# Performance work log

Hardware: AMD Instinct MI355X
Metric: run time of the kernel (lower is better)

Reference implementation:

```python
import jax, jax.numpy as jnp
import numpy as np

N = 50000
E = 400000
IN_DIM = 128
HID = 128
OUT = 128
HEADS = 4
NEG_SLOPE = 0.2
EPS = 1e-16


def setup_inputs() -> dict:
    key = jax.random.key(0)
    ks = jax.random.split(key, 12)
    s = 0.05
    return {
        "x": jax.random.normal(ks[0], (N, IN_DIM), dtype=jnp.float32),
        "edge_index": jax.random.randint(ks[1], (2, E), 0, N, dtype=jnp.int64),
        # layer 1: in_dim -> hid, heads=4, concat
        "W1": jax.random.normal(ks[2], (IN_DIM, HEADS * HID), dtype=jnp.float32) * s,
        "att_src1": jax.random.normal(ks[3], (HEADS, HID), dtype=jnp.float32) * s,
        "att_dst1": jax.random.normal(ks[4], (HEADS, HID), dtype=jnp.float32) * s,
        "bias1": jnp.zeros((HEADS * HID,), dtype=jnp.float32),
        # layer 2: hid*heads -> out, heads=1, no concat
        "W2": jax.random.normal(ks[5], (HEADS * HID, OUT), dtype=jnp.float32) * s,
        "att_src2": jax.random.normal(ks[6], (1, OUT), dtype=jnp.float32) * s,
        "att_dst2": jax.random.normal(ks[7], (1, OUT), dtype=jnp.float32) * s,
        "bias2": jnp.zeros((OUT,), dtype=jnp.float32),
    }


def gat_conv(x, src, dst, W, att_src, att_dst, bias, heads, out_dim, concat):
    n = x.shape[0]
    h = (x @ W).reshape(n, heads, out_dim)                       # [N,H,D]
    a_src = jnp.sum(h * att_src[None], axis=-1)                  # [N,H]
    a_dst = jnp.sum(h * att_dst[None], axis=-1)                  # [N,H]
    e = jax.nn.leaky_relu(a_src[src] + a_dst[dst], NEG_SLOPE)    # [E,H]
    # segment softmax over incoming edges of each dst node
    e_max = jax.ops.segment_max(e, dst, num_segments=n)          # [N,H]
    ex = jnp.exp(e - e_max[dst])
    denom = jax.ops.segment_sum(ex, dst, num_segments=n)         # [N,H]
    alpha = ex / (denom[dst] + EPS)                              # [E,H]
    msg = h[src] * alpha[..., None]                              # [E,H,D]
    out = jax.ops.segment_sum(msg, dst, num_segments=n)          # [N,H,D]
    out = out.reshape(n, heads * out_dim) if concat else out.mean(axis=1)
    return out + bias


def reference(x, edge_index, W1, att_src1, att_dst1, bias1, W2, att_src2, att_dst2, bias2):
    n = x.shape[0]
    loop = jnp.arange(n, dtype=edge_index.dtype)
    src = jnp.concatenate([edge_index[0], loop])  # PyG add_self_loops=True
    dst = jnp.concatenate([edge_index[1], loop])
    h = jax.nn.elu(gat_conv(x, src, dst, W1, att_src1, att_dst1, bias1, HEADS, HID, True))
    z = jax.nn.elu(gat_conv(h, src, dst, W2, att_src2, att_dst2, bias2, 1, OUT, False))
    # F.normalize(z, dim=-1): L2 with eps=1e-12 clamp on the norm
    norm = jnp.maximum(jnp.linalg.norm(z, axis=-1, keepdims=True), 1e-12)
    return z / norm
```

## Files before the change

kernel.cpp:

```cpp
#include <hip/hip_runtime.h>
#include <cstddef>

#define N_NODES 50000
#define N_EDGES 400000
#define TOT_EDGES (N_EDGES + N_NODES)
#define M_PAD 50048
#define SCAN_PAD 50176
#define NBLK 49
#define CNT_BLKS 1758

typedef _Float16 f16;
typedef __attribute__((ext_vector_type(8))) _Float16 f16x8;
typedef __attribute__((ext_vector_type(4))) _Float16 f16x4;
typedef __attribute__((ext_vector_type(2))) _Float16 f16x2;
typedef __attribute__((ext_vector_type(4))) float f32x4;

__device__ __forceinline__ float lrelu(float e) { return e > 0.f ? e : 0.2f * e; }

__global__ void zero_int(int* __restrict__ p, int n) {
  int i = blockIdx.x * blockDim.x + threadIdx.x;
  if (i < n) p[i] = 0;
}

__global__ __launch_bounds__(256) void count_weights(
    const int* __restrict__ ei, int* __restrict__ deg,
    const float* __restrict__ W1, const float* __restrict__ W2,
    const float* __restrict__ att_s1, const float* __restrict__ att_d1,
    const float* __restrict__ att_s2, const float* __restrict__ att_d2,
    f16* __restrict__ w1t, f16* __restrict__ w2t,
    float* __restrict__ V1s, float* __restrict__ V1d,
    float* __restrict__ V2s, float* __restrict__ V2d) {
  const int b = blockIdx.x;
  if (b < CNT_BLKS) {
    const int e = b * 256 + threadIdx.x;
    if (e >= TOT_EDGES) return;
    const int dst = (e < N_EDGES) ? ei[N_EDGES + e] : (e - N_EDGES);
    atomicAdd(&deg[dst], 1);
    return;
  }
  const int bb = b - CNT_BLKS;
  if (bb < 256) {
    const int idx = bb * 256 + threadIdx.x;
    const int cc = idx >> 7, rr = idx & 127;
    w1t[idx] = (f16)W1[(size_t)rr * 512 + cc];
  } else if (bb < 512) {
    const int idx = (bb - 256) * 256 + threadIdx.x;
    const int cc = idx >> 9, rr = idx & 511;
    w2t[idx] = (f16)W2[(size_t)rr * 128 + cc];
  } else if (bb < 640) {
    const int wid = (bb - 512) * 4 + (threadIdx.x >> 6);
    const int lane = threadIdx.x & 63;
    const int k = wid >> 2, h = wid & 3;
    const float* wrow = W1 + (size_t)k * 512 + h * 128;
    float2 wv = *(const float2*)&wrow[lane * 2];
    float2 sv = *(const float2*)&att_s1[h * 128 + lane * 2];
    float2 dv = *(const float2*)&att_d1[h * 128 + lane * 2];
    float ps = wv.x * sv.x + wv.y * sv.y;
    float pd = wv.x * dv.x + wv.y * dv.y;
#pragma unroll
    for (int off = 32; off; off >>= 1) {
      ps += __shfl_xor(ps, off);
      pd += __shfl_xor(pd, off);
    }
    if (lane == 0) { V1s[k * 4 + h] = ps; V1d[k * 4 + h] = pd; }
  } else {
    const int wid = (bb - 640) * 4 + (threadIdx.x >> 6);
    const int lane = threadIdx.x & 63;
    const float* wrow = W2 + (size_t)wid * 128;
    float2 wv = *(const float2*)&wrow[lane * 2];
    float2 sv = *(const float2*)&att_s2[lane * 2];
    float2 dv = *(const float2*)&att_d2[lane * 2];
    float ps = wv.x * sv.x + wv.y * sv.y;
    float pd = wv.x * dv.x + wv.y * dv.y;
#pragma unroll
    for (int off = 32; off; off >>= 1) {
      ps += __shfl_xor(ps, off);
      pd += __shfl_xor(pd, off);
    }
    if (lane == 0) { V2s[wid] = ps; V2d[wid] = pd; }
  }
}

__global__ __launch_bounds__(256) void histscan_prepx(
    const int* __restrict__ deg, int* __restrict__ pre, int* __restrict__ bsum,
    int* __restrict__ blkcnt,
    const float* __restrict__ x, f16* __restrict__ xb,
    const float* __restrict__ V1s, const float* __restrict__ V1d,
    float* __restrict__ as1, float* __restrict__ ad1, f16* __restrict__ aggb) {
  __shared__ int wsum[4];
  __shared__ int lh[128];
  const int b = blockIdx.x;
  if (b < NBLK) {
    const int t = threadIdx.x, lane = t & 63, w = t >> 6;
    if (t < 128) lh[t] = 0;
    __syncthreads();
    const int base = b * 1024 + t * 4;
    int4 v = *(const int4*)&deg[base];
    if (base + 0 < N_NODES) atomicAdd(&lh[min(v.x, 127)], 1);
    if (base + 1 < N_NODES) atomicAdd(&lh[min(v.y, 127)], 1);
    if (base + 2 < N_NODES) atomicAdd(&lh[min(v.z, 127)], 1);
    if (base + 3 < N_NODES) atomicAdd(&lh[min(v.w, 127)], 1);
    const int s = v.x + v.y + v.z + v.w;
    int xx = s;
#pragma unroll
    for (int off = 1; off < 64; off <<= 1) {
      int y = __shfl_up(xx, off);
      if (lane >= off) xx += y;
    }
    if (lane == 63) wsum[w] = xx;
    __syncthreads();
    int woff = 0;
    for (int j = 0; j < w; ++j) woff += wsum[j];
    const int ex = xx - s + woff;
    pre[base + 0] = ex;
    pre[base + 1] = ex + v.x;
    pre[base + 2] = ex + v.x + v.y;
    pre[base + 3] = ex + v.x + v.y + v.z;
    if (t == 255) bsum[b] = ex + s;
    if (t < 128) blkcnt[t * NBLK + b] = lh[t];
    return;
  }
  const int wid = (b - NBLK) * 4 + (threadIdx.x >> 6);
  const int lane = threadIdx.x & 63;
  const int k = lane * 2;
  if (wid >= N_NODES) {
    f16x2 z; z[0] = (f16)0.f; z[1] = (f16)0.f;
    *(f16x2*)&xb[(size_t)wid * 128 + k] = z;
    f16x8 z8;
#pragma unroll
    for (int j = 0; j < 8; ++j) z8[j] = (f16)0.f;
    *(f16x8*)&aggb[(size_t)wid * 512 + lane * 8] = z8;
    return;
  }
  float2 xv = *(const float2*)&x[(size_t)wid * 128 + k];
  f16x2 o; o[0] = (f16)xv.x; o[1] = (f16)xv.y;
  *(f16x2*)&xb[(size_t)wid * 128 + k] = o;
  float4 vs0 = *(const float4*)&V1s[k * 4];
  float4 vs1 = *(const float4*)&V1s[(k + 1) * 4];
  float4 vd0 = *(const float4*)&V1d[k * 4];
  float4 vd1 = *(const float4*)&V1d[(k + 1) * 4];
  float s[4], d[4];
  s[0] = xv.x * vs0.x + xv.y * vs1.x;
  s[1] = xv.x * vs0.y + xv.y * vs1.y;
  s[2] = xv.x * vs0.z + xv.y * vs1.z;
  s[3] = xv.x * vs0.w + xv.y * vs1.w;
  d[0] = xv.x * vd0.x + xv.y * vd1.x;
  d[1] = xv.x * vd0.y + xv.y * vd1.y;
  d[2] = xv.x * vd0.z + xv.y * vd1.z;
  d[3] = xv.x * vd0.w + xv.y * vd1.w;
#pragma unroll
  for (int h = 0; h < 4; ++h) {
#pragma unroll
    for (int off = 32; off; off >>= 1) {
      s[h] += __shfl_xor(s[h], off);
      d[h] += __shfl_xor(d[h], off);
    }
  }
  if (lane == 0) {
    *(float4*)&as1[(size_t)wid * 4] = make_float4(s[0], s[1], s[2], s[3]);
    *(float4*)&ad1[(size_t)wid * 4] = make_float4(d[0], d[1], d[2], d[3]);
  }
}

__global__ __launch_bounds__(128) void scan2(int* __restrict__ bsum,
                                             const int* __restrict__ blkcnt,
                                             int* __restrict__ boff) {
  __shared__ int tot[128];
  const int t = threadIdx.x;
  int s = 0;
  for (int k = 0; k < NBLK; ++k) s += blkcnt[t * NBLK + k];
  tot[t] = s;
  __syncthreads();
  if (t == 0) {
    int acc = 0;
    for (int b = 0; b < 128; ++b) { const int v = tot[b]; tot[b] = acc; acc += v; }
  }
  __syncthreads();
  int acc = tot[t];
  for (int k = 0; k < NBLK; ++k) {
    boff[t * NBLK + k] = acc;
    acc += blkcnt[t * NBLK + k];
  }
  if (t < 64) {
    int v = (t < NBLK) ? bsum[t] : 0;
    int xx = v;
#pragma unroll
    for (int off = 1; off < 64; off <<= 1) {
      int y = __shfl_up(xx, off);
      if (t >= off) xx += y;
    }
    if (t < NBLK) bsum[t] = xx - v;
  }
}

__global__ __launch_bounds__(256) void scatter_addoff(
    int* __restrict__ pre, const int* __restrict__ bsumoff,
    int* __restrict__ cursor, const int* __restrict__ deg,
    const int* __restrict__ boff, int* __restrict__ order) {
  __shared__ int lcur[128];
  const int t = threadIdx.x;
  const int b = blockIdx.x;
  if (t < 128) lcur[t] = boff[t * NBLK + b];
  __syncthreads();
  const int base4 = b * 1024 + t * 4;
  const int off = bsumoff[b];
  int4 v = *(const int4*)&pre[base4];
  v.x += off; v.y += off; v.z += off; v.w += off;
  *(int4*)&pre[base4] = v;
  *(int4*)&cursor[base4] = v;
#pragma unroll
  for (int j = 0; j < 4; ++j) {
    const int i = b * 1024 + j * 256 + t;
    if (i < N_NODES) {
      const int bk = min(deg[i], 127);
      const int pos = atomicAdd(&lcur[bk], 1);
      order[pos] = i;
    }
  }
}

__global__ void fill_w1(const int* __restrict__ ei, int* __restrict__ cursor,
                        const float* __restrict__ as1, const float* __restrict__ ad1,
                        int* __restrict__ csr, float* __restrict__ wexp1) {
  const int e = blockIdx.x * blockDim.x + threadIdx.x;
  if (e >= TOT_EDGES) return;
  int s, d;
  if (e < N_EDGES) { s = ei[e]; d = ei[N_EDGES + e]; }
  else             { s = d = e - N_EDGES; }
  const int pos = atomicAdd(&cursor[d], 1);
  csr[pos] = s;
  float4 a = *(const float4*)&as1[(size_t)s * 4];
  float4 bz = *(const float4*)&ad1[(size_t)d * 4];
  float4 w;
  w.x = __expf(lrelu(a.x + bz.x));
  w.y = __expf(lrelu(a.y + bz.y));
  w.z = __expf(lrelu(a.z + bz.z));
  w.w = __expf(lrelu(a.w + bz.w));
  *(float4*)&wexp1[(size_t)pos * 4] = w;
}

template <int K, bool PER_HEAD, bool FUSE_A2>
__global__ __launch_bounds__(256) void gemm_bt(const f16* __restrict__ A, int lda,
                                               const f16* __restrict__ Bt, int ldb,
                                               f16* __restrict__ C, int ldc,
                                               const float* __restrict__ bias,
                                               const float* __restrict__ V2s,
                                               const float* __restrict__ V2d,
                                               float* __restrict__ as2,
                                               float* __restrict__ ad2) {
  if constexpr (PER_HEAD) {
    const int hh = blockIdx.y;
    A += (size_t)hh * 128;
    Bt += (size_t)hh * 128 * 128;
    C += (size_t)hh * 128;
    bias += hh * 128;
  }
  constexpr int LDT = 72;
  __shared__ __align__(16) f16 As[128 * LDT];
  __shared__ __align__(16) f16 Bs[128 * LDT];
  const int tid = threadIdx.x;
  const int lane = tid & 63;
  const int g = lane >> 4, r16 = lane & 15;
  const int w = tid >> 6, wr = w >> 1, wc = w & 1;
  const long bm = (long)blockIdx.x * 128;

  const int row0 = tid >> 2, h0 = tid & 3;
  const int p1 = (h0 & 1) * 16 + (h0 >> 1) * 4;
  const size_t ga0 = (size_t)(bm + row0) * lda + h0 * 8;
  const size_t ga1 = (size_t)(bm + row0 + 64) * lda + h0 * 8;
  const size_t gb0 = (size_t)row0 * ldb + h0 * 8;
  const size_t gb1 = (size_t)(row0 + 64) * ldb + h0 * 8;
  const int la0 = row0 * LDT + p1, la1 = (row0 + 64) * LDT + p1;

  f32x4 acc[4][4] = {};
  float s2a = 0.f, d2a = 0.f, s2b = 0.f, d2b = 0.f;

  for (int k0 = 0; k0 < K; k0 += 64) {
    __syncthreads();
    f16x8 a0k0 = *(const f16x8*)&A[ga0 + k0];
    f16x8 a0k1 = *(const f16x8*)&A[ga0 + k0 + 32];
    f16x8 a1k0 = *(const f16x8*)&A[ga1 + k0];
    f16x8 a1k1 = *(const f16x8*)&A[ga1 + k0 + 32];
    f16x8 b0k0 = *(const f16x8*)&Bt[gb0 + k0];
    f16x8 b0k1 = *(const f16x8*)&Bt[gb0 + k0 + 32];
    f16x8 b1k0 = *(const f16x8*)&Bt[gb1 + k0];
    f16x8 b1k1 = *(const f16x8*)&Bt[gb1 + k0 + 32];
    if constexpr (FUSE_A2) {
#pragma unroll
      for (int c = 0; c < 2; ++c) {
        const int kc = k0 + c * 32 + h0 * 8;
        const f16x8 va = c ? a0k1 : a0k0;
        const f16x8 vb = c ? a1k1 : a1k0;
        float4 vsa = *(const float4*)&V2s[kc];
        float4 vsb = *(const float4*)&V2s[kc + 4];
        float4 vda = *(const float4*)&V2d[kc];
        float4 vdb = *(const float4*)&V2d[kc + 4];
        const float vs[8] = {vsa.x, vsa.y, vsa.z, vsa.w, vsb.x, vsb.y, vsb.z, vsb.w};
        const float vd[8] = {vda.x, vda.y, vda.z, vda.w, vdb.x, vdb.y, vdb.z, vdb.w};
#pragma unroll
        for (int j = 0; j < 8; ++j) {
          s2a += (float)va[j] * vs[j];
          d2a += (float)va[j] * vd[j];
          s2b += (float)vb[j] * vs[j];
          d2b += (float)vb[j] * vd[j];
        }
      }
    }
    *(f16x4*)&As[la0]      = __builtin_shufflevector(a0k0, a0k0, 0, 1, 2, 3);
    *(f16x4*)&As[la0 + 8]  = __builtin_shufflevector(a0k0, a0k0, 4, 5, 6, 7);
    *(f16x4*)&As[la0 + 32] = __builtin_shufflevector(a0k1, a0k1, 0, 1, 2, 3);
    *(f16x4*)&As[la0 + 40] = __builtin_shufflevector(a0k1, a0k1, 4, 5, 6, 7);
    *(f16x4*)&As[la1]      = __builtin_shufflevector(a1k0, a1k0, 0, 1, 2, 3);
    *(f16x4*)&As[la1 + 8]  = __builtin_shufflevector(a1k0, a1k0, 4, 5, 6, 7);
    *(f16x4*)&As[la1 + 32] = __builtin_shufflevector(a1k1, a1k1, 0, 1, 2, 3);
    *(f16x4*)&As[la1 + 40] = __builtin_shufflevector(a1k1, a1k1, 4, 5, 6, 7);
    *(f16x4*)&Bs[la0]      = __builtin_shufflevector(b0k0, b0k0, 0, 1, 2, 3);
    *(f16x4*)&Bs[la0 + 8]  = __builtin_shufflevector(b0k0, b0k0, 4, 5, 6, 7);
    *(f16x4*)&Bs[la0 + 32] = __builtin_shufflevector(b0k1, b0k1, 0, 1, 2, 3);
    *(f16x4*)&Bs[la0 + 40] = __builtin_shufflevector(b0k1, b0k1, 4, 5, 6, 7);
    *(f16x4*)&Bs[la1]      = __builtin_shufflevector(b1k0, b1k0, 0, 1, 2, 3);
    *(f16x4*)&Bs[la1 + 8]  = __builtin_shufflevector(b1k0, b1k0, 4, 5, 6, 7);
    *(f16x4*)&Bs[la1 + 32] = __builtin_shufflevector(b1k1, b1k1, 0, 1, 2, 3);
    *(f16x4*)&Bs[la1 + 40] = __builtin_shufflevector(b1k1, b1k1, 4, 5, 6, 7);
    __syncthreads();
#pragma unroll
    for (int ks = 0; ks < 2; ++ks) {
      f16x8 af[4], bfv[4];
#pragma unroll
      for (int m = 0; m < 4; ++m)
        af[m] = *(const f16x8*)&As[(wr * 64 + m * 16 + r16) * LDT + ks * 32 + g * 8];
#pragma unroll
      for (int n = 0; n < 4; ++n)
        bfv[n] = *(const f16x8*)&Bs[(wc * 64 + n * 16 + r16) * LDT + ks * 32 + g * 8];
#pragma unroll
      for (int m = 0; m < 4; ++m)
#pragma unroll
        for (int n = 0; n < 4; ++n)
          acc[m][n] = __builtin_amdgcn_mfma_f32_16x16x32_f16(af[m], bfv[n], acc[m][n], 0, 0, 0);
    }
  }

  if constexpr (FUSE_A2) {
    s2a += __shfl_xor(s2a, 1); s2a += __shfl_xor(s2a, 2);
    d2a += __shfl_xor(d2a, 1); d2a += __shfl_xor(d2a, 2);
    s2b += __shfl_xor(s2b, 1); s2b += __shfl_xor(s2b, 2);
    d2b += __shfl_xor(d2b, 1); d2b += __shfl_xor(d2b, 2);
    if ((tid & 3) == 0) {
      const long r0 = bm + row0;
      as2[r0] = s2a; ad2[r0] = d2a;
      as2[r0 + 64] = s2b; ad2[r0 + 64] = d2b;
    }
  }

#pragma unroll
  for (int m = 0; m < 4; ++m) {
#pragma unroll
    for (int n = 0; n < 4; ++n) {
      const long row = bm + wr * 64 + m * 16 + g * 4;
      const int col = wc * 64 + n * 16 + r16;
      float bv = 0.f;
      if constexpr (PER_HEAD) bv = bias[col];
#pragma unroll
      for (int r = 0; r < 4; ++r) {
        float v = acc[m][n][r];
        if constexpr (PER_HEAD) {
          v += bv;
          v = v > 0.f ? v : (__expf(v) - 1.f);
        }
        C[(size_t)(row + r) * ldc + col] = (f16)v;
      }
    }
  }
}

__global__ __launch_bounds__(256) void aggregate1x(
    const f16* __restrict__ xsrc, const float* __restrict__ wexp,
    const int* __restrict__ rowstart, const int* __restrict__ csr,
    const int* __restrict__ order, f16* __restrict__ aggb) {
  const int wave = (blockIdx.x * blockDim.x + threadIdx.x) >> 6;
  const int lane = threadIdx.x & 63;
  const int g16 = lane >> 4, l16 = lane & 15;
  const int node = order[N_NODES - 1 - (wave * 4 + g16)];
  const int col0 = l16 * 8;
  const int rs = rowstart[node];
  const int re = rowstart[node + 1];
  const int deg = re - rs;

  int maxdeg = deg, mindeg = deg;
  maxdeg = max(maxdeg, __shfl_xor(maxdeg, 16));
  maxdeg = max(maxdeg, __shfl_xor(maxdeg, 32));
  mindeg = min(mindeg, __shfl_xor(mindeg, 16));
  mindeg = min(mindeg, __shfl_xor(mindeg, 32));

  constexpr int D = 4;
  int sreg[D];
  float4 wreg[D];
  f16x8 hreg[D];
#pragma unroll
  for (int p = 0; p < D; ++p) {
    const int k = rs + p;
    const int kc = (k < re) ? k : (re - 1);
    wreg[p] = *(const float4*)&wexp[(size_t)kc * 4];
    const int s = csr[kc];
    hreg[p] = *(const f16x8*)&xsrc[(size_t)s * 128 + col0];
    const int k2 = rs + D + p;
    sreg[p] = csr[(k2 < re) ? k2 : (re - 1)];
  }

  float acc0[8] = {}, acc1[8] = {}, acc2[8] = {}, acc3[8] = {};
  float Z0 = 0.f, Z1 = 0.f, Z2 = 0.f, Z3 = 0.f;

  int base = 0;
  for (; base + D <= mindeg; base += D) {
#pragma unroll
    for (int p = 0; p < D; ++p) {
      const int i = base + p;
      const float4 wv = wreg[p];
      const f16x8 h = hreg[p];
      const int nk = rs + i + D;
      if (nk < re) {
        wreg[p] = *(const float4*)&wexp[(size_t)nk * 4];
        const int s = sreg[p];
        hreg[p] = *(const f16x8*)&xsrc[(size_t)s * 128 + col0];
      }
      const int nk2 = rs + i + 2 * D;
      if (nk2 < re) sreg[p] = csr[nk2];
      Z0 += wv.x; Z1 += wv.y; Z2 += wv.z; Z3 += wv.w;
#pragma unroll
      for (int j = 0; j < 8; ++j) {
        const float hv = (float)h[j];
        acc0[j] += wv.x * hv;
        acc1[j] += wv.y * hv;
        acc2[j] += wv.z * hv;
        acc3[j] += wv.w * hv;
      }
    }
  }
  for (; base < maxdeg; base += D) {
#pragma unroll
    for (int p = 0; p < D; ++p) {
      const int i = base + p;
      const bool act = i < deg;
      const float4 wv = wreg[p];
      const float w0 = act ? wv.x : 0.f;
      const float w1 = act ? wv.y : 0.f;
      const float w2 = act ? wv.z : 0.f;
      const float w3 = act ? wv.w : 0.f;
      const f16x8 h = hreg[p];
      const int nk = rs + i + D;
      if (nk < re) {
        wreg[p] = *(const float4*)&wexp[(size_t)nk * 4];
        const int s = sreg[p];
        hreg[p] = *(const f16x8*)&xsrc[(size_t)s * 128 + col0];
      }
      const int nk2 = rs + i + 2 * D;
      if (nk2 < re) sreg[p] = csr[nk2];
      Z0 += w0; Z1 += w1; Z2 += w2; Z3 += w3;
#pragma unroll
      for (int j = 0; j < 8; ++j) {
        const float hv = (float)h[j];
        acc0[j] += w0 * hv;
        acc1[j] += w1 * hv;
        acc2[j] += w2 * hv;
        acc3[j] += w3 * hv;
      }
    }
  }

  const float i0 = 1.f / (Z0 + 1e-16f);
  const float i1 = 1.f / (Z1 + 1e-16f);
  const float i2 = 1.f / (Z2 + 1e-16f);
  const float i3 = 1.f / (Z3 + 1e-16f);
  f16* orow = aggb + (size_t)node * 512 + col0;
  f16x8 o0, o1, o2, o3;
#pragma unroll
  for (int j = 0; j < 8; ++j) {
    o0[j] = (f16)(acc0[j] * i0);
    o1[j] = (f16)(acc1[j] * i1);
    o2[j] = (f16)(acc2[j] * i2);
    o3[j] = (f16)(acc3[j] * i3);
  }
  *(f16x8*)&orow[0]   = o0;
  *(f16x8*)&orow[128] = o1;
  *(f16x8*)&orow[256] = o2;
  *(f16x8*)&orow[384] = o3;
}

__global__ __launch_bounds__(256) void aggregate2(
    const f16* __restrict__ hsrc, const float* __restrict__ as2,
    const float* __restrict__ ad2, const int* __restrict__ rowstart,
    const int* __restrict__ csr, const int* __restrict__ order,
    const float* __restrict__ bias, float* __restrict__ out) {
  const int wave = (blockIdx.x * blockDim.x + threadIdx.x) >> 6;
  const int lane = threadIdx.x & 63;
  const int g16 = lane >> 4, l16 = lane & 15;
  const int node = order[N_NODES - 1 - (wave * 4 + g16)];
  const int col0 = l16 * 8;
  const int rs = rowstart[node];
  const int re = rowstart[node + 1];
  const int deg = re - rs;
  const float ad = ad2[node];

  int maxdeg = deg, mindeg = deg;
  maxdeg = max(maxdeg, __shfl_xor(maxdeg, 16));
  maxdeg = max(maxdeg, __shfl_xor(maxdeg, 32));
  mindeg = min(mindeg, __shfl_xor(mindeg, 16));
  mindeg = min(mindeg, __shfl_xor(mindeg, 32));

  constexpr int D = 6;
  int sreg[D];
  float areg[D];
  f16x8 hreg[D];
#pragma unroll
  for (int p = 0; p < D; ++p) {
    const int k = rs + p;
    const int kc = (k < re) ? k : (re - 1);
    const int s = csr[kc];
    areg[p] = as2[s];
    hreg[p] = *(const f16x8*)&hsrc[(size_t)s * 128 + col0];
    const int k2 = rs + D + p;
    sreg[p] = csr[(k2 < re) ? k2 : (re - 1)];
  }

  float acc[8] = {};
  float Z = 0.f;
  int base = 0;
  for (; base + D <= mindeg; base += D) {
#pragma unroll
    for (int p = 0; p < D; ++p) {
      const int i = base + p;
      const float w = __expf(lrelu(areg[p] + ad));
      const f16x8 h = hreg[p];
      const int nk = rs + i + D;
      if (nk < re) {
        const int s = sreg[p];
        areg[p] = as2[s];
        hreg[p] = *(const f16x8*)&hsrc[(size_t)s * 128 + col0];
      }
      const int nk2 = rs + i + 2 * D;
      if (nk2 < re) sreg[p] = csr[nk2];
      Z += w;
#pragma unroll
      for (int j = 0; j < 8; ++j) acc[j] += w * (float)h[j];
    }
  }
  for (; base < maxdeg; base += D) {
#pragma unroll
    for (int p = 0; p < D; ++p) {
      const int i = base + p;
      const bool act = i < deg;
      const float w = act ? __expf(lrelu(areg[p] + ad)) : 0.f;
      const f16x8 h = hreg[p];
      const int nk = rs + i + D;
      if (nk < re) {
        const int s = sreg[p];
        areg[p] = as2[s];
        hreg[p] = *(const f16x8*)&hsrc[(size_t)s * 128 + col0];
      }
      const int nk2 = rs + i + 2 * D;
      if (nk2 < re) sreg[p] = csr[nk2];
      Z += w;
#pragma unroll
      for (int j = 0; j < 8; ++j) acc[j] += w * (float)h[j];
    }
  }
  const float inv = 1.f / (Z + 1e-16f);

  float4 ba = *(const float4*)&bias[col0];
  float4 bb = *(const float4*)&bias[col0 + 4];
  const float bv[8] = {ba.x, ba.y, ba.z, ba.w, bb.x, bb.y, bb.z, bb.w};
  float v[8];
  float ss = 0.f;
#pragma unroll
  for (int j = 0; j < 8; ++j) {
    float t = acc[j] * inv + bv[j];
    t = t > 0.f ? t : (__expf(t) - 1.f);
    v[j] = t;
    ss += t * t;
  }
  ss += __shfl_xor(ss, 1);
  ss += __shfl_xor(ss, 2);
  ss += __shfl_xor(ss, 4);
  ss += __shfl_xor(ss, 8);
  const float invn = 1.f / fmaxf(sqrtf(ss), 1e-12f);
  float* orow = out + (size_t)node * 128 + col0;
  float4 oa = make_float4(v[0] * invn, v[1] * invn, v[2] * invn, v[3] * invn);
  float4 ob = make_float4(v[4] * invn, v[5] * invn, v[6] * invn, v[7] * invn);
  *(float4*)&orow[0] = oa;
  *(float4*)&orow[4] = ob;
}

extern "C" void kernel_launch(void* const* d_in, const int* in_sizes, int n_in,
                              void* d_out, int out_size, void* d_ws, size_t ws_size,
                              hipStream_t stream) {
  const float* x        = (const float*)d_in[0];
  const int*   ei       = (const int*)d_in[1];
  const float* W1       = (const float*)d_in[2];
  const float* att_src1 = (const float*)d_in[3];
  const float* att_dst1 = (const float*)d_in[4];
  const float* bias1    = (const float*)d_in[5];
  const float* W2       = (const float*)d_in[6];
  const float* att_src2 = (const float*)d_in[7];
  const float* att_dst2 = (const float*)d_in[8];
  const float* bias2    = (const float*)d_in[9];
  float* out = (float*)d_out;

  char* ws = (char*)d_ws;
  size_t off = 0;
  auto alloc = [&](size_t bytes) {
    char* p = ws + off;
    off = (off + bytes + 255) & ~(size_t)255;
    return p;
  };
  f16* xb    = (f16*)alloc(sizeof(f16) * (size_t)M_PAD * 128);
  f16* w1t   = (f16*)alloc(sizeof(f16) * 512 * 128);
  f16* w2t   = (f16*)alloc(sizeof(f16) * 128 * 512);
  f16* aggb  = (f16*)alloc(sizeof(f16) * (size_t)M_PAD * 512);
  f16* out1b = (f16*)alloc(sizeof(f16) * (size_t)M_PAD * 512);
  float* V1s = (float*)alloc(sizeof(float) * 512);
  float* V1d = (float*)alloc(sizeof(float) * 512);
  float* V2s = (float*)alloc(sizeof(float) * 512);
  float* V2d = (float*)alloc(sizeof(float) * 512);
  float* as1 = (float*)alloc(sizeof(float) * N_NODES * 4);
  float* ad1 = (float*)alloc(sizeof(float) * N_NODES * 4);
  float* as2 = (float*)alloc(sizeof(float) * M_PAD);
  float* ad2 = (float*)alloc(sizeof(float) * M_PAD);
  float* wexp1 = (float*)alloc(sizeof(float) * (size_t)TOT_EDGES * 4);
  int* rowstart = (int*)alloc(sizeof(int) * (SCAN_PAD + 4));
  int* deg      = (int*)alloc(sizeof(int) * SCAN_PAD);
  int* cursor   = (int*)alloc(sizeof(int) * SCAN_PAD);
  int* bsum     = (int*)alloc(sizeof(int) * 64);
  int* blkcnt   = (int*)alloc(sizeof(int) * 128 * NBLK);
  int* boff     = (int*)alloc(sizeof(int) * 128 * NBLK);
  int* order    = (int*)alloc(sizeof(int) * N_NODES);
  int* csr      = (int*)alloc(sizeof(int) * TOT_EDGES);
  f16* h2b = aggb;

  const int agrid = (N_NODES / 4) * 64 / 256;

  zero_int<<<(SCAN_PAD + 255) / 256, 256, 0, stream>>>(deg, SCAN_PAD);
  count_weights<<<CNT_BLKS + 768, 256, 0, stream>>>(
      ei, deg, W1, W2, att_src1, att_dst1, att_src2, att_dst2,
      w1t, w2t, V1s, V1d, V2s, V2d);
  histscan_prepx<<<NBLK + M_PAD / 4, 256, 0, stream>>>(
      deg, rowstart, bsum, blkcnt, x, xb, V1s, V1d, as1, ad1, aggb);
  scan2<<<1, 128, 0, stream>>>(bsum, blkcnt, boff);
  scatter_addoff<<<NBLK, 256, 0, stream>>>(rowstart, bsum, cursor, deg, boff, order);
  fill_w1<<<CNT_BLKS, 256, 0, stream>>>(ei, cursor, as1, ad1, csr, wexp1);
  aggregate1x<<<agrid, 256, 0, stream>>>(xb, wexp1, rowstart, csr, order, aggb);
  gemm_bt<128, true, false><<<dim3(M_PAD / 128, 4), 256, 0, stream>>>(
      aggb, 512, w1t, 128, out1b, 512, bias1, nullptr, nullptr, nullptr, nullptr);
  gemm_bt<512, false, true><<<dim3(M_PAD / 128, 1), 256, 0, stream>>>(
      out1b, 512, w2t, 512, h2b, 128, nullptr, V2s, V2d, as2, ad2);
  aggregate2<<<agrid, 256, 0, stream>>>(h2b, as2, ad2, rowstart, csr, order, bias2, out);
}
```

Baseline: 192.1 us.

## Fuse the two GEMMs into one kernel and merge scan into scatter

```diff
diff --git a/kernel.cpp b/kernel.cpp
--- a/kernel.cpp
+++ b/kernel.cpp
@@ -11,7 +11,6 @@
 
 typedef _Float16 f16;
 typedef __attribute__((ext_vector_type(8))) _Float16 f16x8;
-typedef __attribute__((ext_vector_type(4))) _Float16 f16x4;
 typedef __attribute__((ext_vector_type(2))) _Float16 f16x2;
 typedef __attribute__((ext_vector_type(4))) float f32x4;
 
@@ -162,48 +161,40 @@
   }
 }
 
-__global__ __launch_bounds__(128) void scan2(int* __restrict__ bsum,
-                                             const int* __restrict__ blkcnt,
-                                             int* __restrict__ boff) {
-  __shared__ int tot[128];
-  const int t = threadIdx.x;
-  int s = 0;
-  for (int k = 0; k < NBLK; ++k) s += blkcnt[t * NBLK + k];
-  tot[t] = s;
-  __syncthreads();
-  if (t == 0) {
-    int acc = 0;
-    for (int b = 0; b < 128; ++b) { const int v = tot[b]; tot[b] = acc; acc += v; }
-  }
-  __syncthreads();
-  int acc = tot[t];
-  for (int k = 0; k < NBLK; ++k) {
-    boff[t * NBLK + k] = acc;
-    acc += blkcnt[t * NBLK + k];
-  }
-  if (t < 64) {
-    int v = (t < NBLK) ? bsum[t] : 0;
-    int xx = v;
-#pragma unroll
-    for (int off = 1; off < 64; off <<= 1) {
-      int y = __shfl_up(xx, off);
-      if (t >= off) xx += y;
-    }
-    if (t < NBLK) bsum[t] = xx - v;
-  }
-}
-
-__global__ __launch_bounds__(256) void scatter_addoff(
-    int* __restrict__ pre, const int* __restrict__ bsumoff,
+__global__ __launch_bounds__(256) void scatter_addoff2(
+    int* __restrict__ pre, const int* __restrict__ bsum,
     int* __restrict__ cursor, const int* __restrict__ deg,
-    const int* __restrict__ boff, int* __restrict__ order) {
+    const int* __restrict__ blkcnt, int* __restrict__ order) {
   __shared__ int lcur[128];
+  __shared__ int carry_s;
+  __shared__ int boff_s;
   const int t = threadIdx.x;
   const int b = blockIdx.x;
-  if (t < 128) lcur[t] = boff[t * NBLK + b];
+  int x = 0, tot = 0, pre_b = 0;
+  if (t < 128) {
+    for (int k = 0; k < NBLK; ++k) {
+      const int v = blkcnt[t * NBLK + k];
+      tot += v;
+      if (k < b) pre_b += v;
+    }
+    x = tot;
+#pragma unroll
+    for (int off = 1; off < 64; off <<= 1) {
+      int y = __shfl_up(x, off);
+      if ((t & 63) >= off) x += y;
+    }
+  }
+  if (t == 63) carry_s = x;
+  if (t == 255) {
+    int s = 0;
+    for (int k = 0; k < b; ++k) s += bsum[k];
+    boff_s = s;
+  }
+  __syncthreads();
+  if (t < 128) lcur[t] = (x - tot) + (t >= 64 ? carry_s : 0) + pre_b;
   __syncthreads();
   const int base4 = b * 1024 + t * 4;
-  const int off = bsumoff[b];
+  const int off = boff_s;
   int4 v = *(const int4*)&pre[base4];
   v.x += off; v.y += off; v.z += off; v.w += off;
   *(int4*)&pre[base4] = v;
@@ -239,138 +230,140 @@
   *(float4*)&wexp1[(size_t)pos * 4] = w;
 }
 
-template <int K, bool PER_HEAD, bool FUSE_A2>
-__global__ __launch_bounds__(256) void gemm_bt(const f16* __restrict__ A, int lda,
-                                               const f16* __restrict__ Bt, int ldb,
-                                               f16* __restrict__ C, int ldc,
-                                               const float* __restrict__ bias,
-                                               const float* __restrict__ V2s,
-                                               const float* __restrict__ V2d,
-                                               float* __restrict__ as2,
-                                               float* __restrict__ ad2) {
-  if constexpr (PER_HEAD) {
-    const int hh = blockIdx.y;
-    A += (size_t)hh * 128;
-    Bt += (size_t)hh * 128 * 128;
-    C += (size_t)hh * 128;
-    bias += hh * 128;
-  }
-  constexpr int LDT = 72;
-  __shared__ __align__(16) f16 As[128 * LDT];
-  __shared__ __align__(16) f16 Bs[128 * LDT];
+#define GLDT 72
+#define C1LD 136
+
+__global__ __launch_bounds__(256) void fused_mlp(
+    const f16* __restrict__ aggb, const f16* __restrict__ w1t,
+    const f16* __restrict__ w2t, const float* __restrict__ bias1,
+    const float* __restrict__ V2s, const float* __restrict__ V2d,
+    f16* __restrict__ h2b, float* __restrict__ as2, float* __restrict__ ad2) {
+  __shared__ __align__(16) f16 As[128 * GLDT];
+  __shared__ __align__(16) f16 Bs[128 * GLDT];
+  __shared__ __align__(16) f16 C1s[128 * C1LD];
+  __shared__ float a2sl[128], a2dl[128];
   const int tid = threadIdx.x;
   const int lane = tid & 63;
   const int g = lane >> 4, r16 = lane & 15;
   const int w = tid >> 6, wr = w >> 1, wc = w & 1;
-  const long bm = (long)blockIdx.x * 128;
-
+  const size_t bm = (size_t)blockIdx.x * 128;
   const int row0 = tid >> 2, h0 = tid & 3;
-  const int p1 = (h0 & 1) * 16 + (h0 >> 1) * 4;
-  const size_t ga0 = (size_t)(bm + row0) * lda + h0 * 8;
-  const size_t ga1 = (size_t)(bm + row0 + 64) * lda + h0 * 8;
-  const size_t gb0 = (size_t)row0 * ldb + h0 * 8;
-  const size_t gb1 = (size_t)(row0 + 64) * ldb + h0 * 8;
-  const int la0 = row0 * LDT + p1, la1 = (row0 + 64) * LDT + p1;
-
-  f32x4 acc[4][4] = {};
-  float s2a = 0.f, d2a = 0.f, s2b = 0.f, d2b = 0.f;
-
-  for (int k0 = 0; k0 < K; k0 += 64) {
-    __syncthreads();
-    f16x8 a0k0 = *(const f16x8*)&A[ga0 + k0];
-    f16x8 a0k1 = *(const f16x8*)&A[ga0 + k0 + 32];
-    f16x8 a1k0 = *(const f16x8*)&A[ga1 + k0];
-    f16x8 a1k1 = *(const f16x8*)&A[ga1 + k0 + 32];
-    f16x8 b0k0 = *(const f16x8*)&Bt[gb0 + k0];
-    f16x8 b0k1 = *(const f16x8*)&Bt[gb0 + k0 + 32];
-    f16x8 b1k0 = *(const f16x8*)&Bt[gb1 + k0];
-    f16x8 b1k1 = *(const f16x8*)&Bt[gb1 + k0 + 32];
-    if constexpr (FUSE_A2) {
-#pragma unroll
-      for (int c = 0; c < 2; ++c) {
-        const int kc = k0 + c * 32 + h0 * 8;
-        const f16x8 va = c ? a0k1 : a0k0;
-        const f16x8 vb = c ? a1k1 : a1k0;
-        float4 vsa = *(const float4*)&V2s[kc];
-        float4 vsb = *(const float4*)&V2s[kc + 4];
-        float4 vda = *(const float4*)&V2d[kc];
-        float4 vdb = *(const float4*)&V2d[kc + 4];
-        const float vs[8] = {vsa.x, vsa.y, vsa.z, vsa.w, vsb.x, vsb.y, vsb.z, vsb.w};
-        const float vd[8] = {vda.x, vda.y, vda.z, vda.w, vdb.x, vdb.y, vdb.z, vdb.w};
-#pragma unroll
-        for (int j = 0; j < 8; ++j) {
-          s2a += (float)va[j] * vs[j];
-          d2a += (float)va[j] * vd[j];
-          s2b += (float)vb[j] * vs[j];
-          d2b += (float)vb[j] * vd[j];
+
+  if (tid < 128) { a2sl[tid] = 0.f; a2dl[tid] = 0.f; }
+
+  f32x4 acc2[4][4] = {};
+
+  for (int h = 0; h < 4; ++h) {
+    f32x4 acc1[4][4] = {};
+    const f16* Ag = aggb + (size_t)h * 128;
+    const f16* Bg = w1t + (size_t)h * 128 * 128;
+#pragma unroll
+    for (int k0 = 0; k0 < 128; k0 += 64) {
+      __syncthreads();
+      f16x8 a00 = *(const f16x8*)&Ag[(bm + row0) * 512 + k0 + h0 * 8];
+      f16x8 a01 = *(const f16x8*)&Ag[(bm + row0) * 512 + k0 + 32 + h0 * 8];
+      f16x8 a10 = *(const f16x8*)&Ag[(bm + row0 + 64) * 512 + k0 + h0 * 8];
+      f16x8 a11 = *(const f16x8*)&Ag[(bm + row0 + 64) * 512 + k0 + 32 + h0 * 8];
+      f16x8 b00 = *(const f16x8*)&Bg[row0 * 128 + k0 + h0 * 8];
+      f16x8 b01 = *(const f16x8*)&Bg[row0 * 128 + k0 + 32 + h0 * 8];
+      f16x8 b10 = *(const f16x8*)&Bg[(row0 + 64) * 128 + k0 + h0 * 8];
+      f16x8 b11 = *(const f16x8*)&Bg[(row0 + 64) * 128 + k0 + 32 + h0 * 8];
+      *(f16x8*)&As[row0 * GLDT + h0 * 8] = a00;
+      *(f16x8*)&As[row0 * GLDT + 32 + h0 * 8] = a01;
+      *(f16x8*)&As[(row0 + 64) * GLDT + h0 * 8] = a10;
+      *(f16x8*)&As[(row0 + 64) * GLDT + 32 + h0 * 8] = a11;
+      *(f16x8*)&Bs[row0 * GLDT + h0 * 8] = b00;
+      *(f16x8*)&Bs[row0 * GLDT + 32 + h0 * 8] = b01;
+      *(f16x8*)&Bs[(row0 + 64) * GLDT + h0 * 8] = b10;
+      *(f16x8*)&Bs[(row0 + 64) * GLDT + 32 + h0 * 8] = b11;
+      __syncthreads();
+#pragma unroll
+      for (int ks = 0; ks < 2; ++ks) {
+        f16x8 af[4], bf[4];
+#pragma unroll
+        for (int m = 0; m < 4; ++m)
+          af[m] = *(const f16x8*)&As[(wr * 64 + m * 16 + r16) * GLDT + ks * 32 + g * 8];
+#pragma unroll
+        for (int n = 0; n < 4; ++n)
+          bf[n] = *(const f16x8*)&Bs[(wc * 64 + n * 16 + r16) * GLDT + ks * 32 + g * 8];
+#pragma unroll
+        for (int m = 0; m < 4; ++m)
+#pragma unroll
+          for (int n = 0; n < 4; ++n)
+            acc1[m][n] = __builtin_amdgcn_mfma_f32_16x16x32_f16(af[m], bf[n], acc1[m][n], 0, 0, 0);
+      }
+    }
+    float bv[4], vsv[4], vdv[4];
+#pragma unroll
+    for (int n = 0; n < 4; ++n) {
+      const int c = h * 128 + wc * 64 + n * 16 + r16;
+      bv[n] = bias1[c];
+      vsv[n] = V2s[c];
+      vdv[n] = V2d[c];
+    }
+#pragma unroll
+    for (int m = 0; m < 4; ++m) {
+#pragma unroll
+      for (int r = 0; r < 4; ++r) {
+        const int rl = wr * 64 + m * 16 + g * 4 + r;
+        float sp = 0.f, dp = 0.f;
+#pragma unroll
+        for (int n = 0; n < 4; ++n) {
+          float v = acc1[m][n][r] + bv[n];
+          v = v > 0.f ? v : (__expf(v) - 1.f);
+          C1s[rl * C1LD + wc * 64 + n * 16 + r16] = (f16)v;
+          sp += v * vsv[n];
+          dp += v * vdv[n];
         }
-      }
-    }
-    *(f16x4*)&As[la0]      = __builtin_shufflevector(a0k0, a0k0, 0, 1, 2, 3);
-    *(f16x4*)&As[la0 + 8]  = __builtin_shufflevector(a0k0, a0k0, 4, 5, 6, 7);
-    *(f16x4*)&As[la0 + 32] = __builtin_shufflevector(a0k1, a0k1, 0, 1, 2, 3);
-    *(f16x4*)&As[la0 + 40] = __builtin_shufflevector(a0k1, a0k1, 4, 5, 6, 7);
-    *(f16x4*)&As[la1]      = __builtin_shufflevector(a1k0, a1k0, 0, 1, 2, 3);
-    *(f16x4*)&As[la1 + 8]  = __builtin_shufflevector(a1k0, a1k0, 4, 5, 6, 7);
-    *(f16x4*)&As[la1 + 32] = __builtin_shufflevector(a1k1, a1k1, 0, 1, 2, 3);
-    *(f16x4*)&As[la1 + 40] = __builtin_shufflevector(a1k1, a1k1, 4, 5, 6, 7);
-    *(f16x4*)&Bs[la0]      = __builtin_shufflevector(b0k0, b0k0, 0, 1, 2, 3);
-    *(f16x4*)&Bs[la0 + 8]  = __builtin_shufflevector(b0k0, b0k0, 4, 5, 6, 7);
-    *(f16x4*)&Bs[la0 + 32] = __builtin_shufflevector(b0k1, b0k1, 0, 1, 2, 3);
-    *(f16x4*)&Bs[la0 + 40] = __builtin_shufflevector(b0k1, b0k1, 4, 5, 6, 7);
-    *(f16x4*)&Bs[la1]      = __builtin_shufflevector(b1k0, b1k0, 0, 1, 2, 3);
-    *(f16x4*)&Bs[la1 + 8]  = __builtin_shufflevector(b1k0, b1k0, 4, 5, 6, 7);
-    *(f16x4*)&Bs[la1 + 32] = __builtin_shufflevector(b1k1, b1k1, 0, 1, 2, 3);
-    *(f16x4*)&Bs[la1 + 40] = __builtin_shufflevector(b1k1, b1k1, 4, 5, 6, 7);
-    __syncthreads();
-#pragma unroll
-    for (int ks = 0; ks < 2; ++ks) {
-      f16x8 af[4], bfv[4];
-#pragma unroll
-      for (int m = 0; m < 4; ++m)
-        af[m] = *(const f16x8*)&As[(wr * 64 + m * 16 + r16) * LDT + ks * 32 + g * 8];
-#pragma unroll
-      for (int n = 0; n < 4; ++n)
-        bfv[n] = *(const f16x8*)&Bs[(wc * 64 + n * 16 + r16) * LDT + ks * 32 + g * 8];
-#pragma unroll
-      for (int m = 0; m < 4; ++m)
+        atomicAdd(&a2sl[rl], sp);
+        atomicAdd(&a2dl[rl], dp);
+      }
+    }
+    const f16* B2g = w2t + (size_t)h * 128;
+#pragma unroll
+    for (int k0 = 0; k0 < 128; k0 += 64) {
+      __syncthreads();
+      f16x8 b00 = *(const f16x8*)&B2g[(size_t)row0 * 512 + k0 + h0 * 8];
+      f16x8 b01 = *(const f16x8*)&B2g[(size_t)row0 * 512 + k0 + 32 + h0 * 8];
+      f16x8 b10 = *(const f16x8*)&B2g[(size_t)(row0 + 64) * 512 + k0 + h0 * 8];
+      f16x8 b11 = *(const f16x8*)&B2g[(size_t)(row0 + 64) * 512 + k0 + 32 + h0 * 8];
+      *(f16x8*)&Bs[row0 * GLDT + h0 * 8] = b00;
+      *(f16x8*)&Bs[row0 * GLDT + 32 + h0 * 8] = b01;
+      *(f16x8*)&Bs[(row0 + 64) * GLDT + h0 * 8] = b10;
+      *(f16x8*)&Bs[(row0 + 64) * GLDT + 32 + h0 * 8] = b11;
+      __syncthreads();
+#pragma unroll
+      for (int ks = 0; ks < 2; ++ks) {
+        f16x8 af[4], bf[4];
+#pragma unroll
+        for (int m = 0; m < 4; ++m)
+          af[m] = *(const f16x8*)&C1s[(wr * 64 + m * 16 + r16) * C1LD + k0 + ks * 32 + g * 8];
 #pragma unroll
         for (int n = 0; n < 4; ++n)
-          acc[m][n] = __builtin_amdgcn_mfma_f32_16x16x32_f16(af[m], bfv[n], acc[m][n], 0, 0, 0);
-    }
-  }
-
-  if constexpr (FUSE_A2) {
-    s2a += __shfl_xor(s2a, 1); s2a += __shfl_xor(s2a, 2);
-    d2a += __shfl_xor(d2a, 1); d2a += __shfl_xor(d2a, 2);
-    s2b += __shfl_xor(s2b, 1); s2b += __shfl_xor(s2b, 2);
-    d2b += __shfl_xor(d2b, 1); d2b += __shfl_xor(d2b, 2);
-    if ((tid & 3) == 0) {
-      const long r0 = bm + row0;
-      as2[r0] = s2a; ad2[r0] = d2a;
-      as2[r0 + 64] = s2b; ad2[r0 + 64] = d2b;
-    }
-  }
-
-#pragma unroll
-  for (int m = 0; m < 4; ++m) {
+          bf[n] = *(const f16x8*)&Bs[(wc * 64 + n * 16 + r16) * GLDT + ks * 32 + g * 8];
+#pragma unroll
+        for (int m = 0; m < 4; ++m)
+#pragma unroll
+          for (int n = 0; n < 4; ++n)
+            acc2[m][n] = __builtin_amdgcn_mfma_f32_16x16x32_f16(af[m], bf[n], acc2[m][n], 0, 0, 0);
+      }
+    }
+  }
+  __syncthreads();
+  if (tid < 128) {
+    as2[bm + tid] = a2sl[tid];
+    ad2[bm + tid] = a2dl[tid];
+  }
+#pragma unroll
+  for (int m = 0; m < 4; ++m)
 #pragma unroll
     for (int n = 0; n < 4; ++n) {
-      const long row = bm + wr * 64 + m * 16 + g * 4;
+      const size_t row = bm + wr * 64 + m * 16 + g * 4;
       const int col = wc * 64 + n * 16 + r16;
-      float bv = 0.f;
-      if constexpr (PER_HEAD) bv = bias[col];
-#pragma unroll
-      for (int r = 0; r < 4; ++r) {
-        float v = acc[m][n][r];
-        if constexpr (PER_HEAD) {
-          v += bv;
-          v = v > 0.f ? v : (__expf(v) - 1.f);
-        }
-        C[(size_t)(row + r) * ldc + col] = (f16)v;
-      }
-    }
-  }
+#pragma unroll
+      for (int r = 0; r < 4; ++r)
+        h2b[(row + r) * 128 + col] = (f16)acc2[m][n][r];
+    }
 }
 
 __global__ __launch_bounds__(256) void aggregate1x(
@@ -616,7 +609,7 @@
   f16* w1t   = (f16*)alloc(sizeof(f16) * 512 * 128);
   f16* w2t   = (f16*)alloc(sizeof(f16) * 128 * 512);
   f16* aggb  = (f16*)alloc(sizeof(f16) * (size_t)M_PAD * 512);
-  f16* out1b = (f16*)alloc(sizeof(f16) * (size_t)M_PAD * 512);
+  f16* h2b   = (f16*)alloc(sizeof(f16) * (size_t)M_PAD * 128);
   float* V1s = (float*)alloc(sizeof(float) * 512);
   float* V1d = (float*)alloc(sizeof(float) * 512);
   float* V2s = (float*)alloc(sizeof(float) * 512);
@@ -631,10 +624,8 @@
   int* cursor   = (int*)alloc(sizeof(int) * SCAN_PAD);
   int* bsum     = (int*)alloc(sizeof(int) * 64);
   int* blkcnt   = (int*)alloc(sizeof(int) * 128 * NBLK);
-  int* boff     = (int*)alloc(sizeof(int) * 128 * NBLK);
   int* order    = (int*)alloc(sizeof(int) * N_NODES);
   int* csr      = (int*)alloc(sizeof(int) * TOT_EDGES);
-  f16* h2b = aggb;
 
   const int agrid = (N_NODES / 4) * 64 / 256;
 
@@ -644,13 +635,10 @@
       w1t, w2t, V1s, V1d, V2s, V2d);
   histscan_prepx<<<NBLK + M_PAD / 4, 256, 0, stream>>>(
       deg, rowstart, bsum, blkcnt, x, xb, V1s, V1d, as1, ad1, aggb);
-  scan2<<<1, 128, 0, stream>>>(bsum, blkcnt, boff);
-  scatter_addoff<<<NBLK, 256, 0, stream>>>(rowstart, bsum, cursor, deg, boff, order);
+  scatter_addoff2<<<NBLK, 256, 0, stream>>>(rowstart, bsum, cursor, deg, blkcnt, order);
   fill_w1<<<CNT_BLKS, 256, 0, stream>>>(ei, cursor, as1, ad1, csr, wexp1);
   aggregate1x<<<agrid, 256, 0, stream>>>(xb, wexp1, rowstart, csr, order, aggb);
-  gemm_bt<128, true, false><<<dim3(M_PAD / 128, 4), 256, 0, stream>>>(
-      aggb, 512, w1t, 128, out1b, 512, bias1, nullptr, nullptr, nullptr, nullptr);
-  gemm_bt<512, false, true><<<dim3(M_PAD / 128, 1), 256, 0, stream>>>(
-      out1b, 512, w2t, 512, h2b, 128, nullptr, V2s, V2d, as2, ad2);
+  fused_mlp<<<M_PAD / 128, 256, 0, stream>>>(
+      aggb, w1t, w2t, bias1, V2s, V2d, h2b, as2, ad2);
   aggregate2<<<agrid, 256, 0, stream>>>(h2b, as2, ad2, rowstart, csr, order, bias2, out);
 }
```

After: 278.7 us. 45.1% more time.
